# Kernel tuning notes

Hardware: AMD Instinct MI355X
Metric: run time of the kernel (lower is better)

## Reference

```python
import jax, jax.numpy as jnp
import numpy as np

N_NODES = 10000
N_EDGES = 160000
F_IN = 128
F_OUT = 128
BATCH = 8


def setup_inputs() -> dict:
    key = jax.random.key(0)
    k1, k2, k3, k4 = jax.random.split(key, 4)
    scale = 1.0 / np.sqrt(F_IN)
    x = jax.random.normal(k1, (BATCH, N_NODES, F_IN), dtype=jnp.float32)
    W_l = jax.random.normal(k2, (F_OUT, F_IN), dtype=jnp.float32) * scale
    b_l = jnp.zeros((F_OUT,), dtype=jnp.float32)
    W_r = jax.random.normal(k3, (F_OUT, F_IN), dtype=jnp.float32) * scale
    edge_index = jax.random.randint(k4, (2, N_EDGES), 0, N_NODES, dtype=jnp.int64)
    return {"x": x, "W_l": W_l, "b_l": b_l, "W_r": W_r, "edge_index": edge_index}


def reference(x, W_l, b_l, W_r, edge_index):
    # SAGEConv (PyG, mean aggr): out_i = W_l @ mean_{j->i} x_j + b_l + W_r @ x_i
    src = edge_index[0]  # message source nodes
    dst = edge_index[1]  # message target nodes
    deg = jax.ops.segment_sum(jnp.ones((src.shape[0],), x.dtype), dst,
                              num_segments=N_NODES)  # [N]
    deg = jnp.maximum(deg, 1.0)[:, None]  # avoid div-by-zero

    def agg_one(xs):  # xs: [N, F]
        msgs = xs[src]  # [E, F] gather
        return jax.ops.segment_sum(msgs, dst, num_segments=N_NODES) / deg

    mean_nbr = jax.vmap(agg_one)(x)  # [B, N, F]
    out = jnp.einsum('bnf,of->bno', mean_nbr, W_l) + b_l \
        + jnp.einsum('bnf,of->bno', x, W_r)
    return out
```

## Files before the change

### kernel.cpp

```cpp
#include <hip/hip_runtime.h>
#include <hip/hip_bf16.h>

#define N_NODES 10000
#define N_EDGES 160000
#define F_IN    128
#define F_OUT   128
#define BATCH   8
#define NROWS   (BATCH * N_NODES)
#define NT      8

#define WS_FLAG_OFF   0
#define WS_WT_OFF     256
#define WS_DEG_OFF    131328
#define WS_ROW_OFF    171328
#define WS_CUR_OFF    211332
#define WS_COL_OFF    251332
#define WS_TOTAL      891332

#define WS2_FLAG  0
#define WS2_WT    256
#define WS2_DEG   65792
#define WS2_ROW   105792
#define WS2_CUR   145796
#define WS2_COL   185796
#define WS2_XH    825856
#define WS2_NEED  21305856

typedef __attribute__((ext_vector_type(8))) short short8;
typedef __attribute__((ext_vector_type(4))) float floatx4;

__device__ __forceinline__ int edge_val(const void* ei, int idx, int i64) {
    if (i64) return (int)((const long long*)ei)[idx];
    return ((const int*)ei)[idx];
}

__global__ void detect_i64_kernel(const void* ei, int* flag) {
    __shared__ int any_nonzero;
    if (threadIdx.x == 0) any_nonzero = 0;
    __syncthreads();
    int v = ((const int*)ei)[2 * threadIdx.x + 1];
    if (v != 0) atomicOr(&any_nonzero, 1);
    __syncthreads();
    if (threadIdx.x == 0) *flag = (any_nonzero == 0) ? 1 : 0;
}

__global__ void hist_kernel(const void* ei, const int* __restrict__ flag,
                            int* __restrict__ deg) {
    int e = blockIdx.x * 256 + threadIdx.x;
    if (e >= N_EDGES) return;
    int i64 = *flag;
    int d = edge_val(ei, N_EDGES + e, i64);
    atomicAdd(&deg[d], 1);
}

__global__ __launch_bounds__(1024)
void scan_kernel(const int* __restrict__ deg, int* __restrict__ row_start) {
    __shared__ int sd[1024];
    const int CH = (N_NODES + 1023) / 1024;
    int t = threadIdx.x;
    int beg = t * CH;
    int end = min(N_NODES, beg + CH);
    int s = 0;
    for (int i = beg; i < end; i++) s += deg[i];
    sd[t] = s;
    __syncthreads();
    for (int off = 1; off < 1024; off <<= 1) {
        int v = (t >= off) ? sd[t - off] : 0;
        __syncthreads();
        sd[t] += v;
        __syncthreads();
    }
    int run = sd[t] - s;
    for (int i = beg; i < end; i++) { row_start[i] = run; run += deg[i]; }
    if (t == 1023) row_start[N_NODES] = sd[1023];
}

__global__ void scatter_kernel(const void* ei, const int* __restrict__ flag,
                               const int* __restrict__ row_start,
                               int* __restrict__ cursor, int* __restrict__ col) {
    int e = blockIdx.x * 256 + threadIdx.x;
    if (e >= N_EDGES) return;
    int i64 = *flag;
    int s = edge_val(ei, e, i64);
    int d = edge_val(ei, N_EDGES + e, i64);
    int pos = atomicAdd(&cursor[d], 1);
    col[row_start[d] + pos] = s;
}


__device__ __forceinline__ unsigned short f2bf(float v) {
    __hip_bfloat16 h = __float2bfloat16(v);
    return *(unsigned short*)&h;
}

__device__ __forceinline__ uint2 pack4(float4 v) {
    uint2 r;
    r.x = (unsigned)f2bf(v.x) | ((unsigned)f2bf(v.y) << 16);
    r.y = (unsigned)f2bf(v.z) | ((unsigned)f2bf(v.w) << 16);
    return r;
}

__device__ __forceinline__ void acc4(float4& a, uint2 p) {
    a.x += __uint_as_float(p.x << 16);
    a.y += __uint_as_float(p.x & 0xffff0000u);
    a.z += __uint_as_float(p.y << 16);
    a.w += __uint_as_float(p.y & 0xffff0000u);
}

__global__ void make_wt_bf16(const float* __restrict__ Wl,
                             const float* __restrict__ Wr,
                             unsigned short* __restrict__ Wt) {
    int idx = blockIdx.x * 256 + threadIdx.x;
    int o = idx >> 8;
    int k = idx & 255;
    float v = (k < F_IN) ? Wl[o * F_IN + k] : Wr[o * F_IN + (k - F_IN)];
    Wt[idx] = f2bf(v);
}

__global__ __launch_bounds__(256)
void convert_kernel(const float* __restrict__ x, uint2* __restrict__ xh2) {
    int t = blockIdx.x * 256 + threadIdx.x;
    float4 v = ((const float4*)x)[t];
    xh2[t] = pack4(v);
}

__global__ __launch_bounds__(256)
void sage_fused_mfma(const uint2* __restrict__ xh2,
                     const int* __restrict__ row_start,
                     const int* __restrict__ col,
                     const unsigned short* __restrict__ Wt,
                     const float* __restrict__ bl,
                     float* __restrict__ out) {
    __shared__ unsigned short Z[64 * 256];

    const int n0 = blockIdx.x * NT;
    const int t  = threadIdx.x;
    const int b  = t >> 5;
    const int c  = t & 31;

    const size_t bbase = (size_t)b * N_NODES;

    #pragma unroll 2
    for (int ni = 0; ni < NT; ++ni) {
        const int n   = n0 + ni;
        const int beg = row_start[n];
        const int end = row_start[n + 1];
        const int d   = end - beg;

        float4 s0 = make_float4(0.f,0.f,0.f,0.f), s1 = s0, s2 = s0, s3 = s0;
        int i = beg;
        for (; i + 4 <= end; i += 4) {
            int m0 = col[i], m1 = col[i+1], m2 = col[i+2], m3 = col[i+3];
            acc4(s0, xh2[(bbase + m0) * 32 + c]);
            acc4(s1, xh2[(bbase + m1) * 32 + c]);
            acc4(s2, xh2[(bbase + m2) * 32 + c]);
            acc4(s3, xh2[(bbase + m3) * 32 + c]);
        }
        for (; i < end; ++i) acc4(s0, xh2[(bbase + col[i]) * 32 + c]);

        s0.x += s1.x + s2.x + s3.x; s0.y += s1.y + s2.y + s3.y;
        s0.z += s1.z + s2.z + s3.z; s0.w += s1.w + s2.w + s3.w;
        const float inv = 1.0f / (float)max(d, 1);
        uint2 mp = pack4(make_float4(s0.x*inv, s0.y*inv, s0.z*inv, s0.w*inv));
        uint2 sp = xh2[(bbase + n) * 32 + c];

        const int r   = b * 8 + ni;
        const int sub = (c & 1) * 8;
        const int cc0 = c >> 1;
        const int cc1 = 16 + (c >> 1);
        *(uint2*)((char*)Z + r * 512 + ((cc0 ^ (r & 7)) * 16) + sub) = mp;
        *(uint2*)((char*)Z + r * 512 + ((cc1 ^ (r & 7)) * 16) + sub) = sp;
    }
    __syncthreads();

    const int w  = t >> 6;
    const int l  = t & 63;
    const int lr = l & 15;
    const int kg = l >> 4;

    floatx4 acc[8];
    #pragma unroll
    for (int j = 0; j < 8; ++j) acc[j] = (floatx4){0.f, 0.f, 0.f, 0.f};

    #pragma unroll
    for (int ks = 0; ks < 8; ++ks) {
        const int r   = w * 16 + lr;
        const int cch = ks * 4 + kg;
        short8 af = *(const short8*)((const char*)Z + r * 512 + ((cch ^ (r & 7)) * 16));
        #pragma unroll
        for (int jt = 0; jt < 8; ++jt) {
            short8 bf = *(const short8*)(Wt + (size_t)(jt * 16 + lr) * 256 + ks * 32 + kg * 8);
            acc[jt] = __builtin_amdgcn_mfma_f32_16x16x32_bf16(af, bf, acc[jt], 0, 0, 0);
        }
    }

    #pragma unroll
    for (int jt = 0; jt < 8; ++jt) {
        const int colo = jt * 16 + lr;
        const float bias = bl[colo];
        const int rt = w * 16 + kg * 4;
        #pragma unroll
        for (int q = 0; q < 4; ++q) {
            const int r = rt + q;
            const int row = (r >> 3) * N_NODES + n0 + (r & 7);
            out[(size_t)row * F_OUT + colo] = acc[jt][q] + bias;
        }
    }
}


__global__ void transpose_w_kernel(const float* __restrict__ Wl,
                                   const float* __restrict__ Wr,
                                   float* __restrict__ Wt) {
    int idx = blockIdx.x * 256 + threadIdx.x;
    int f = idx >> 7;
    int o = idx & 127;
    float v = (f < F_IN) ? Wl[o * F_IN + f] : Wr[o * F_IN + (f - F_IN)];
    Wt[f * F_OUT + o] = v;
}

__global__ __launch_bounds__(256)
void sage_fused_kernel(const float* __restrict__ x,
                       const float* __restrict__ bl,
                       const float* __restrict__ Wt,
                       const int* __restrict__ row_start,
                       const int* __restrict__ col,
                       float* __restrict__ out) {
    __shared__ float in_lds[BATCH][2 * F_IN];

    const int n = blockIdx.x;
    const int t = threadIdx.x;
    const int b = t >> 5;
    const int c = t & 31;

    const int beg = row_start[n];
    const int end = row_start[n + 1];

    const float* xb = x + (size_t)b * N_NODES * F_IN;

    float4 acc = make_float4(0.f, 0.f, 0.f, 0.f);
    for (int i = beg; i < end; i++) {
        int s = col[i];
        const float4 v = *(const float4*)(xb + (size_t)s * F_IN + c * 4);
        acc.x += v.x; acc.y += v.y; acc.z += v.z; acc.w += v.w;
    }
    const float inv = 1.0f / (float)max(end - beg, 1);
    const float4 self = *(const float4*)(xb + (size_t)n * F_IN + c * 4);

    *(float4*)&in_lds[b][c * 4] =
        make_float4(acc.x * inv, acc.y * inv, acc.z * inv, acc.w * inv);
    *(float4*)&in_lds[b][F_IN + c * 4] = self;
    __syncthreads();

    float4 oacc = *(const float4*)(bl + c * 4);
    #pragma unroll 8
    for (int f4 = 0; f4 < 64; f4++) {
        const float4 inq = *(const float4*)&in_lds[b][f4 * 4];
        const float4 w0 = *(const float4*)(Wt + (f4 * 4 + 0) * F_OUT + c * 4);
        const float4 w1 = *(const float4*)(Wt + (f4 * 4 + 1) * F_OUT + c * 4);
        const float4 w2 = *(const float4*)(Wt + (f4 * 4 + 2) * F_OUT + c * 4);
        const float4 w3 = *(const float4*)(Wt + (f4 * 4 + 3) * F_OUT + c * 4);
        oacc.x += inq.x * w0.x; oacc.y += inq.x * w0.y; oacc.z += inq.x * w0.z; oacc.w += inq.x * w0.w;
        oacc.x += inq.y * w1.x; oacc.y += inq.y * w1.y; oacc.z += inq.y * w1.z; oacc.w += inq.y * w1.w;
        oacc.x += inq.z * w2.x; oacc.y += inq.z * w2.y; oacc.z += inq.z * w2.z; oacc.w += inq.z * w2.w;
        oacc.x += inq.w * w3.x; oacc.y += inq.w * w3.y; oacc.z += inq.w * w3.z; oacc.w += inq.w * w3.w;
    }

    *(float4*)(out + ((size_t)b * N_NODES + n) * F_OUT + c * 4) = oacc;
}

extern "C" void kernel_launch(void* const* d_in, const int* in_sizes, int n_in,
                              void* d_out, int out_size, void* d_ws, size_t ws_size,
                              hipStream_t stream) {
    const float* x  = (const float*)d_in[0];
    const float* Wl = (const float*)d_in[1];
    const float* bl = (const float*)d_in[2];
    const float* Wr = (const float*)d_in[3];
    const void*  ei = d_in[4];
    float* out = (float*)d_out;
    char* ws = (char*)d_ws;

    if (ws_size >= (size_t)WS2_NEED + 1024) {
        int*            flag = (int*)(ws + WS2_FLAG);
        unsigned short* Wt   = (unsigned short*)(ws + WS2_WT);
        int*            deg  = (int*)(ws + WS2_DEG);
        int*            rowp = (int*)(ws + WS2_ROW);
        int*            cur  = (int*)(ws + WS2_CUR);
        int*            col  = (int*)(ws + WS2_COL);
        uint2*          xh2  = (uint2*)(ws + WS2_XH);

        hipMemsetAsync(ws + WS2_DEG, 0, WS2_COL - WS2_DEG, stream);
        detect_i64_kernel<<<1, 256, 0, stream>>>(ei, flag);
        make_wt_bf16<<<128, 256, 0, stream>>>(Wl, Wr, Wt);
        hist_kernel<<<(N_EDGES + 255) / 256, 256, 0, stream>>>(ei, flag, deg);
        scan_kernel<<<1, 1024, 0, stream>>>(deg, rowp);
        scatter_kernel<<<(N_EDGES + 255) / 256, 256, 0, stream>>>(ei, flag, rowp, cur, col);
        convert_kernel<<<(NROWS * 32) / 256, 256, 0, stream>>>(x, xh2);
        sage_fused_mfma<<<N_NODES / NT, 256, 0, stream>>>(xh2, rowp, col, Wt, bl, out);
    } else {
        int*   flag      = (int*)(ws + WS_FLAG_OFF);
        float* Wt        = (float*)(ws + WS_WT_OFF);
        int*   deg       = (int*)(ws + WS_DEG_OFF);
        int*   row_start = (int*)(ws + WS_ROW_OFF);
        int*   cursor    = (int*)(ws + WS_CUR_OFF);
        int*   col       = (int*)(ws + WS_COL_OFF);

        hipMemsetAsync(d_ws, 0, WS_TOTAL, stream);
        detect_i64_kernel<<<1, 256, 0, stream>>>(ei, flag);
        transpose_w_kernel<<<(256 * 128) / 256, 256, 0, stream>>>(Wl, Wr, Wt);
        hist_kernel<<<(N_EDGES + 255) / 256, 256, 0, stream>>>(ei, flag, deg);
        scan_kernel<<<1, 1024, 0, stream>>>(deg, row_start);
        scatter_kernel<<<(N_EDGES + 255) / 256, 256, 0, stream>>>(ei, flag, row_start, cursor, col);
        sage_fused_kernel<<<N_NODES, 256, 0, stream>>>(x, bl, Wt, row_start, col, out);
    }
}
```

Measured before the change: 230.6 us.

## Retile fused SAGE kernel to 64 nodes of a single batch per block

Each block now handles 64 consecutive nodes within one batch instead of 8 nodes across all 8 batches, with bounds checks for the final partial tile. This makes adjacency reads and output stores contiguous per block and confines gathers to one batch's feature slice. The aim is better cache locality and write coalescing. Because the batch index comes from the low bits of the block id, neighbouring blocks still touch different batches, which may limit any locality gain.

```diff
diff --git a/kernel.cpp b/kernel.cpp
--- a/kernel.cpp
+++ b/kernel.cpp
@@ -7,7 +7,8 @@
 #define F_OUT   128
 #define BATCH   8
 #define NROWS   (BATCH * N_NODES)
-#define NT      8
+#define TN      64
+#define NTILES  ((N_NODES + TN - 1) / TN)
 
 #define WS_FLAG_OFF   0
 #define WS_WT_OFF     256
@@ -133,19 +134,22 @@
                      float* __restrict__ out) {
     __shared__ unsigned short Z[64 * 256];
 
-    const int n0 = blockIdx.x * NT;
-    const int t  = threadIdx.x;
-    const int b  = t >> 5;
-    const int c  = t & 31;
+    const int b    = blockIdx.x & 7;
+    const int tile = blockIdx.x >> 3;
+    const int n0   = tile * TN;
+    const int t    = threadIdx.x;
+    const int g    = t >> 5;
+    const int c    = t & 31;
 
     const size_t bbase = (size_t)b * N_NODES;
 
     #pragma unroll 2
-    for (int ni = 0; ni < NT; ++ni) {
-        const int n   = n0 + ni;
-        const int beg = row_start[n];
-        const int end = row_start[n + 1];
-        const int d   = end - beg;
+    for (int ni = 0; ni < 8; ++ni) {
+        const int r = ni * 8 + g;
+        const int n = n0 + r;
+        int beg = 0, end = 0;
+        if (n < N_NODES) { beg = row_start[n]; end = row_start[n + 1]; }
+        const int d = end - beg;
 
         float4 s0 = make_float4(0.f,0.f,0.f,0.f), s1 = s0, s2 = s0, s3 = s0;
         int i = beg;
@@ -162,9 +166,9 @@
         s0.z += s1.z + s2.z + s3.z; s0.w += s1.w + s2.w + s3.w;
         const float inv = 1.0f / (float)max(d, 1);
         uint2 mp = pack4(make_float4(s0.x*inv, s0.y*inv, s0.z*inv, s0.w*inv));
-        uint2 sp = xh2[(bbase + n) * 32 + c];
-
-        const int r   = b * 8 + ni;
+        uint2 sp = (n < N_NODES) ? xh2[(bbase + n) * 32 + c]
+                                 : make_uint2(0u, 0u);
+
         const int sub = (c & 1) * 8;
         const int cc0 = c >> 1;
         const int cc1 = 16 + (c >> 1);
@@ -202,8 +206,10 @@
         #pragma unroll
         for (int q = 0; q < 4; ++q) {
             const int r = rt + q;
-            const int row = (r >> 3) * N_NODES + n0 + (r & 7);
-            out[(size_t)row * F_OUT + colo] = acc[jt][q] + bias;
+            const int n = n0 + r;
+            if (n < N_NODES) {
+                out[((size_t)b * N_NODES + n) * F_OUT + colo] = acc[jt][q] + bias;
+            }
         }
     }
 }
@@ -296,7 +302,7 @@
         scan_kernel<<<1, 1024, 0, stream>>>(deg, rowp);
         scatter_kernel<<<(N_EDGES + 255) / 256, 256, 0, stream>>>(ei, flag, rowp, cur, col);
         convert_kernel<<<(NROWS * 32) / 256, 256, 0, stream>>>(x, xh2);
-        sage_fused_mfma<<<N_NODES / NT, 256, 0, stream>>>(xh2, rowp, col, Wt, bl, out);
+        sage_fused_mfma<<<NTILES * BATCH, 256, 0, stream>>>(xh2, rowp, col, Wt, bl, out);
     } else {
         int*   flag      = (int*)(ws + WS_FLAG_OFF);
         float* Wt        = (float*)(ws + WS_WT_OFF);
```

New measurement: 250.5 us. 1.09x slower.

## Shrink fused SAGE block to two nodes with shared-memory neighbor lists

Applied to the files above, without the earlier changes.

Replaces the 8-node-per-block fused gather+MFMA kernel with a 2-node-per-block variant. Each thread now gathers two batch rows per node, and neighbor indices are first staged in LDS. The GEMM is split so each wave computes two output column tiles for the 16 rows, instead of one wave handling 16 rows across all 128 columns. The goal is more blocks for better occupancy and load balance, and less serial per-node looping in the gather. The cost is that each block now rereads the weight matrix for only 16 rows, which is less reuse.

```diff
diff --git a/kernel.cpp b/kernel.cpp
--- a/kernel.cpp
+++ b/kernel.cpp
@@ -7,7 +7,6 @@
 #define F_OUT   128
 #define BATCH   8
 #define NROWS   (BATCH * N_NODES)
-#define NT      8
 
 #define WS_FLAG_OFF   0
 #define WS_WT_OFF     256
@@ -125,52 +124,84 @@
 }
 
 __global__ __launch_bounds__(256)
-void sage_fused_mfma(const uint2* __restrict__ xh2,
-                     const int* __restrict__ row_start,
-                     const int* __restrict__ col,
-                     const unsigned short* __restrict__ Wt,
-                     const float* __restrict__ bl,
-                     float* __restrict__ out) {
-    __shared__ unsigned short Z[64 * 256];
-
-    const int n0 = blockIdx.x * NT;
+void sage_fused2(const uint2* __restrict__ xh2,
+                 const int* __restrict__ row_start,
+                 const int* __restrict__ col,
+                 const unsigned short* __restrict__ Wt,
+                 const float* __restrict__ bl,
+                 float* __restrict__ out) {
+    __shared__ unsigned short Z[16 * 256];
+    __shared__ int nbr[2][1024];
+
+    const int n0 = blockIdx.x * 2;
     const int t  = threadIdx.x;
-    const int b  = t >> 5;
+    const int ni = t >> 7;
+    const int bq = (t >> 5) & 3;
     const int c  = t & 31;
 
-    const size_t bbase = (size_t)b * N_NODES;
-
-    #pragma unroll 2
-    for (int ni = 0; ni < NT; ++ni) {
-        const int n   = n0 + ni;
-        const int beg = row_start[n];
-        const int end = row_start[n + 1];
-        const int d   = end - beg;
-
-        float4 s0 = make_float4(0.f,0.f,0.f,0.f), s1 = s0, s2 = s0, s3 = s0;
-        int i = beg;
-        for (; i + 4 <= end; i += 4) {
-            int m0 = col[i], m1 = col[i+1], m2 = col[i+2], m3 = col[i+3];
-            acc4(s0, xh2[(bbase + m0) * 32 + c]);
-            acc4(s1, xh2[(bbase + m1) * 32 + c]);
-            acc4(s2, xh2[(bbase + m2) * 32 + c]);
-            acc4(s3, xh2[(bbase + m3) * 32 + c]);
-        }
-        for (; i < end; ++i) acc4(s0, xh2[(bbase + col[i]) * 32 + c]);
-
-        s0.x += s1.x + s2.x + s3.x; s0.y += s1.y + s2.y + s3.y;
-        s0.z += s1.z + s2.z + s3.z; s0.w += s1.w + s2.w + s3.w;
-        const float inv = 1.0f / (float)max(d, 1);
-        uint2 mp = pack4(make_float4(s0.x*inv, s0.y*inv, s0.z*inv, s0.w*inv));
-        uint2 sp = xh2[(bbase + n) * 32 + c];
-
-        const int r   = b * 8 + ni;
-        const int sub = (c & 1) * 8;
-        const int cc0 = c >> 1;
-        const int cc1 = 16 + (c >> 1);
-        *(uint2*)((char*)Z + r * 512 + ((cc0 ^ (r & 7)) * 16) + sub) = mp;
-        *(uint2*)((char*)Z + r * 512 + ((cc1 ^ (r & 7)) * 16) + sub) = sp;
-    }
+    const int b0 = row_start[n0];
+    const int e0 = row_start[n0 + 1];
+    const int e1 = row_start[n0 + 2];
+    const int cnt0 = min(e0 - b0, 1024);
+    const int cnt1 = min(e1 - e0, 1024);
+    for (int i = t; i < cnt0; i += 256) nbr[0][i] = col[b0 + i];
+    for (int i = t; i < cnt1; i += 256) nbr[1][i] = col[e0 + i];
+    __syncthreads();
+
+    const int n   = n0 + ni;
+    const int beg = ni ? e0 : b0;
+    const int end = ni ? e1 : e0;
+    const int d   = end - beg;
+    const int cnt = ni ? cnt1 : cnt0;
+    const int* nb = nbr[ni];
+
+    const size_t baseA = (size_t)bq * N_NODES;
+    const size_t baseB = (size_t)(bq + 4) * N_NODES;
+
+    float4 sA0 = make_float4(0.f,0.f,0.f,0.f), sA1 = sA0, sA2 = sA0, sA3 = sA0;
+    float4 sB0 = sA0, sB1 = sA0, sB2 = sA0, sB3 = sA0;
+    int i = 0;
+    for (; i + 4 <= cnt; i += 4) {
+        int m0 = nb[i], m1 = nb[i+1], m2 = nb[i+2], m3 = nb[i+3];
+        acc4(sA0, xh2[(baseA + m0) * 32 + c]);
+        acc4(sB0, xh2[(baseB + m0) * 32 + c]);
+        acc4(sA1, xh2[(baseA + m1) * 32 + c]);
+        acc4(sB1, xh2[(baseB + m1) * 32 + c]);
+        acc4(sA2, xh2[(baseA + m2) * 32 + c]);
+        acc4(sB2, xh2[(baseB + m2) * 32 + c]);
+        acc4(sA3, xh2[(baseA + m3) * 32 + c]);
+        acc4(sB3, xh2[(baseB + m3) * 32 + c]);
+    }
+    for (; i < cnt; ++i) {
+        int m = nb[i];
+        acc4(sA0, xh2[(baseA + m) * 32 + c]);
+        acc4(sB0, xh2[(baseB + m) * 32 + c]);
+    }
+    for (int j = 1024; j < d; ++j) {
+        int m = col[beg + j];
+        acc4(sA0, xh2[(baseA + m) * 32 + c]);
+        acc4(sB0, xh2[(baseB + m) * 32 + c]);
+    }
+    sA0.x += sA1.x + sA2.x + sA3.x; sA0.y += sA1.y + sA2.y + sA3.y;
+    sA0.z += sA1.z + sA2.z + sA3.z; sA0.w += sA1.w + sA2.w + sA3.w;
+    sB0.x += sB1.x + sB2.x + sB3.x; sB0.y += sB1.y + sB2.y + sB3.y;
+    sB0.z += sB1.z + sB2.z + sB3.z; sB0.w += sB1.w + sB2.w + sB3.w;
+
+    const float inv = 1.0f / (float)max(d, 1);
+    uint2 mpA = pack4(make_float4(sA0.x*inv, sA0.y*inv, sA0.z*inv, sA0.w*inv));
+    uint2 mpB = pack4(make_float4(sB0.x*inv, sB0.y*inv, sB0.z*inv, sB0.w*inv));
+    uint2 spA = xh2[(baseA + n) * 32 + c];
+    uint2 spB = xh2[(baseB + n) * 32 + c];
+
+    const int rA  = bq * 2 + ni;
+    const int rB  = (bq + 4) * 2 + ni;
+    const int sub = (c & 1) * 8;
+    const int cc0 = c >> 1;
+    const int cc1 = 16 + (c >> 1);
+    *(uint2*)((char*)Z + rA * 512 + ((cc0 ^ (rA & 7)) * 16) + sub) = mpA;
+    *(uint2*)((char*)Z + rA * 512 + ((cc1 ^ (rA & 7)) * 16) + sub) = spA;
+    *(uint2*)((char*)Z + rB * 512 + ((cc0 ^ (rB & 7)) * 16) + sub) = mpB;
+    *(uint2*)((char*)Z + rB * 512 + ((cc1 ^ (rB & 7)) * 16) + sub) = spB;
     __syncthreads();
 
     const int w  = t >> 6;
@@ -178,32 +209,30 @@
     const int lr = l & 15;
     const int kg = l >> 4;
 
-    floatx4 acc[8];
-    #pragma unroll
-    for (int j = 0; j < 8; ++j) acc[j] = (floatx4){0.f, 0.f, 0.f, 0.f};
+    floatx4 acc0 = (floatx4){0.f, 0.f, 0.f, 0.f};
+    floatx4 acc1 = (floatx4){0.f, 0.f, 0.f, 0.f};
 
     #pragma unroll
     for (int ks = 0; ks < 8; ++ks) {
-        const int r   = w * 16 + lr;
         const int cch = ks * 4 + kg;
-        short8 af = *(const short8*)((const char*)Z + r * 512 + ((cch ^ (r & 7)) * 16));
-        #pragma unroll
-        for (int jt = 0; jt < 8; ++jt) {
-            short8 bf = *(const short8*)(Wt + (size_t)(jt * 16 + lr) * 256 + ks * 32 + kg * 8);
-            acc[jt] = __builtin_amdgcn_mfma_f32_16x16x32_bf16(af, bf, acc[jt], 0, 0, 0);
-        }
+        short8 af = *(const short8*)((const char*)Z + lr * 512 + ((cch ^ (lr & 7)) * 16));
+        short8 bf0 = *(const short8*)(Wt + (size_t)((w * 2 + 0) * 16 + lr) * 256 + ks * 32 + kg * 8);
+        short8 bf1 = *(const short8*)(Wt + (size_t)((w * 2 + 1) * 16 + lr) * 256 + ks * 32 + kg * 8);
+        acc0 = __builtin_amdgcn_mfma_f32_16x16x32_bf16(af, bf0, acc0, 0, 0, 0);
+        acc1 = __builtin_amdgcn_mfma_f32_16x16x32_bf16(af, bf1, acc1, 0, 0, 0);
     }
 
     #pragma unroll
-    for (int jt = 0; jt < 8; ++jt) {
-        const int colo = jt * 16 + lr;
+    for (int jt2 = 0; jt2 < 2; ++jt2) {
+        const int colo = (w * 2 + jt2) * 16 + lr;
         const float bias = bl[colo];
-        const int rt = w * 16 + kg * 4;
+        const floatx4 a = jt2 ? acc1 : acc0;
         #pragma unroll
         for (int q = 0; q < 4; ++q) {
-            const int r = rt + q;
-            const int row = (r >> 3) * N_NODES + n0 + (r & 7);
-            out[(size_t)row * F_OUT + colo] = acc[jt][q] + bias;
+            const int r = kg * 4 + q;
+            const int b = r >> 1;
+            const int nn = n0 + (r & 1);
+            out[((size_t)b * N_NODES + nn) * F_OUT + colo] = a[q] + bias;
         }
     }
 }
@@ -296,7 +325,7 @@
         scan_kernel<<<1, 1024, 0, stream>>>(deg, rowp);
         scatter_kernel<<<(N_EDGES + 255) / 256, 256, 0, stream>>>(ei, flag, rowp, cur, col);
         convert_kernel<<<(NROWS * 32) / 256, 256, 0, stream>>>(x, xh2);
-        sage_fused_mfma<<<N_NODES / NT, 256, 0, stream>>>(xh2, rowp, col, Wt, bl, out);
+        sage_fused2<<<N_NODES / 2, 256, 0, stream>>>(xh2, rowp, col, Wt, bl, out);
     } else {
         int*   flag      = (int*)(ws + WS_FLAG_OFF);
         float* Wt        = (float*)(ws + WS_WT_OFF);
```

After: 205.0 us. -11.1%, faster.
